# Kernel tuning notes

Hardware: AMD Instinct MI355X
Metric: run time of the kernel (lower is better)

## Reference

```python
import jax, jax.numpy as jnp
import numpy as np

B, T, C = 8, 2048, 1024
HEAD_SIZE = 64
HEAD_NUM = 0
NUM_HEADS = 16


def setup_inputs() -> dict:
    key = jax.random.key(0)
    k1, k2, k3, k4 = jax.random.split(key, 4)
    x = jax.random.normal(k1, (B, T, C), dtype=jnp.float32)
    s = C ** -0.5  # Linear init scale
    Wq = jax.random.normal(k2, (C, HEAD_SIZE), dtype=jnp.float32) * s
    Wk = jax.random.normal(k3, (C, HEAD_SIZE), dtype=jnp.float32) * s
    Wv = jax.random.normal(k4, (C, HEAD_SIZE), dtype=jnp.float32) * s
    return {"x": x, "Wq": Wq, "Wk": Wk, "Wv": Wv}


def reference(x, Wq, Wk, Wv):
    # single head of self-attention with ALiBi bias + causal mask (dropout in eval mode = identity)
    q = x @ Wq  # [B,T,H]
    k = x @ Wk  # [B,T,H]
    v = x @ Wv  # [B,T,H]
    scale = jnp.float32(HEAD_SIZE) ** -0.5
    t = jnp.arange(T)
    # base_bias[i,j] = j - i, scaled by per-head ALiBi slope
    slope = 2.0 ** (-8.0 * (HEAD_NUM + 1) / NUM_HEADS)
    m = (t[None, :] - t[:, None]).astype(jnp.float32) * slope  # [T,T]
    # note: bias is added BEFORE the 1/sqrt(d) scaling, as in the original
    scores = (jnp.einsum('bqh,bkh->bqk', q, k) + m) * scale  # [B,T,T]
    causal = t[None, :] <= t[:, None]  # [T,T] lower-triangular
    scores = jnp.where(causal, scores, -jnp.inf)
    attn = jax.nn.softmax(scores, axis=-1)
    out = jnp.einsum('bqk,bkh->bqh', attn, v)  # [B,T,H]
    return out
```

## Files before the change

### kernel.cpp

```cpp
#include <hip/hip_runtime.h>
#include <hip/hip_bf16.h>
#include <math.h>

#define B_ 8
#define T_ 2048
#define C_ 1024
#define H_ 64
#define M_ (B_*T_)

typedef __attribute__((ext_vector_type(8))) short bf16x8;
typedef __attribute__((ext_vector_type(4))) float floatx4;

static __device__ __forceinline__ unsigned short f2bf(float f) {
    union { float f; unsigned u; } v; v.f = f;
    unsigned r = v.u + 0x7fffu + ((v.u >> 16) & 1u);
    return (unsigned short)(r >> 16);
}
static __device__ __forceinline__ unsigned short f2bf_fast(float f) {
    union { float f; unsigned u; } v; v.f = f;
    return (unsigned short)((v.u + 0x8000u) >> 16);
}
static __device__ __forceinline__ unsigned pk2h(float lo, float hi) {
    union { float f; unsigned u; } a, b; a.f = lo; b.f = hi;
    return __builtin_amdgcn_perm(b.u + 0x8000u, a.u + 0x8000u, 0x07060302u);
}
static __device__ __forceinline__ bf16x8 cvt8(float4 f0, float4 f1) {
    union { uint4 u; bf16x8 v; } r;
    r.u.x = pk2h(f0.x, f0.y); r.u.y = pk2h(f0.z, f0.w);
    r.u.z = pk2h(f1.x, f1.y); r.u.w = pk2h(f1.z, f1.w);
    return r.v;
}
static __device__ __forceinline__ float fexp2(float x) {
#if defined(__has_builtin)
#if __has_builtin(__builtin_amdgcn_exp2f)
    return __builtin_amdgcn_exp2f(x);
#else
    return exp2f(x);
#endif
#else
    return exp2f(x);
#endif
}

#define MFMA(a,b,c) __builtin_amdgcn_mfma_f32_16x16x32_bf16((a),(b),(c),0,0,0)

__global__ __launch_bounds__(256) void wprep_kernel(
    const float* __restrict__ Wq, const float* __restrict__ Wk,
    const float* __restrict__ Wv, unsigned short* __restrict__ wt2)
{
    const int f    = blockIdx.x * 256 + threadIdx.x;
    const int nt   = f >> 11;
    const int kc   = (f >> 6) & 31;
    const int lane = f & 63;
    const int l15  = lane & 15, quad = lane >> 4;
    const int col  = nt * 16 + l15;
    const float* W = (col < 64) ? Wq : ((col < 128) ? Wk : Wv);
    const int   cw = col & 63;
    const float sc = (col < 64) ? 0.125f : 1.0f;
    unsigned short o[8];
    #pragma unroll
    for (int j = 0; j < 8; j++) {
        const int kk = kc * 32 + quad * 8 + j;
        o[j] = f2bf(W[(size_t)kk * 64 + cw] * sc);
    }
    *(uint4*)&wt2[(size_t)f * 8] = *(const uint4*)o;
}

__global__ __launch_bounds__(256) void qkv_kernel(
    const float* __restrict__ x, const unsigned short* __restrict__ wt2,
    unsigned short* __restrict__ qo, unsigned short* __restrict__ ko,
    unsigned short* __restrict__ vo)
{
    __shared__ __align__(16) unsigned short smem[32768];

    const int t    = threadIdx.x;
    const int w    = t >> 6;
    const int lane = t & 63;
    const int l15  = lane & 15;
    const int quad = lane >> 4;
    const int r0   = blockIdx.x * 32;

    {
        const int srow = t >> 3;
        const int g0   = t & 7;
        const float* xrow = x + (size_t)(r0 + srow) * C_;
        const int mt_  = srow >> 4;
        const int r15_ = srow & 15;
        const int ks_  = (g0 >> 2) & 1;
        const int qd_  = g0 & 3;
        unsigned short* dst = smem + (ks_ * 2 + mt_) * 512 + (qd_ * 16 + r15_) * 8;

        float4 cA0, cA1, cB0, cB1;
        cA0 = *(const float4*)(xrow + g0 * 8);
        cA1 = *(const float4*)(xrow + g0 * 8 + 4);
        #pragma unroll
        for (int i = 0; i < 16; i++) {
            if (i < 15) {
                cB0 = *(const float4*)(xrow + (i + 1) * 64 + g0 * 8);
                cB1 = *(const float4*)(xrow + (i + 1) * 64 + g0 * 8 + 4);
            }
            *(bf16x8*)(dst + i * 2048) = cvt8(cA0, cA1);
            cA0 = cB0; cA1 = cB1;
        }
    }
    __syncthreads();

    const unsigned short* wb = wt2 + (size_t)(w * 3) * 32 * 512 + lane * 8;

    floatx4 acc[2][3];
    #pragma unroll
    for (int mt = 0; mt < 2; mt++)
        #pragma unroll
        for (int nt = 0; nt < 3; nt++) acc[mt][nt] = (floatx4)(0.0f);

    bf16x8 wcur[6], wnxt[6];
    #pragma unroll
    for (int nt = 0; nt < 3; nt++)
        #pragma unroll
        for (int ks = 0; ks < 2; ks++)
            wcur[nt * 2 + ks] = *(const bf16x8*)(wb + (size_t)(nt * 32 + ks) * 512);

    #pragma unroll 2
    for (int c = 0; c < 16; c++) {
        if (c < 15) {
            #pragma unroll
            for (int nt = 0; nt < 3; nt++)
                #pragma unroll
                for (int ks = 0; ks < 2; ks++)
                    wnxt[nt * 2 + ks] = *(const bf16x8*)
                        (wb + (size_t)(nt * 32 + 2 * (c + 1) + ks) * 512);
        }
        #pragma unroll
        for (int ks = 0; ks < 2; ks++) {
            bf16x8 af[2];
            #pragma unroll
            for (int mt = 0; mt < 2; mt++)
                af[mt] = *(const bf16x8*)
                    (smem + ((c * 2 + ks) * 2 + mt) * 512 + lane * 8);
            #pragma unroll
            for (int mt = 0; mt < 2; mt++)
                #pragma unroll
                for (int nt = 0; nt < 3; nt++)
                    acc[mt][nt] = MFMA(af[mt], wcur[nt * 2 + ks], acc[mt][nt]);
        }
        if (c < 15) {
            #pragma unroll
            for (int i = 0; i < 6; i++) wcur[i] = wnxt[i];
        }
    }

    __syncthreads();
    #pragma unroll
    for (int mt = 0; mt < 2; mt++)
        #pragma unroll
        for (int nt = 0; nt < 3; nt++) {
            const int col = w * 48 + nt * 16 + l15;
            #pragma unroll
            for (int r = 0; r < 4; r++)
                smem[(mt * 16 + quad * 4 + r) * 200 + col] = f2bf(acc[mt][nt][r]);
        }
    __syncthreads();

    {
        const int row = t >> 3;
        const int oct = t & 7;
        *(uint4*)&qo[(size_t)(r0 + row) * 64 + oct * 8] =
            *(const uint4*)&smem[row * 200 + oct * 8];
        *(uint4*)&ko[(size_t)(r0 + row) * 64 + oct * 8] =
            *(const uint4*)&smem[row * 200 + 64 + oct * 8];
    }
    {
        const int h = t >> 2, ts = (t & 3) * 8;
        const int bb = r0 >> 11, tt = r0 & 2047;
        unsigned short tmp[8];
        #pragma unroll
        for (int j = 0; j < 8; j++) tmp[j] = smem[(ts + j) * 200 + 128 + h];
        *(uint4*)&vo[((size_t)bb * 64 + h) * 2048 + tt + ts] = *(uint4*)&tmp[0];
    }
}

#define L2E 1.4426950408889634f
#define BS2 0.12751743f
#define PSTR 76

__global__ __launch_bounds__(256, 3) void attn_kernel(
    const unsigned short* __restrict__ q,
    const unsigned short* __restrict__ k,
    const unsigned short* __restrict__ vT,
    float* __restrict__ out)
{
    __shared__ __align__(16) unsigned char smem[16384 + 512];
    unsigned short* pT  = (unsigned short*)smem;
    float*          Omg = (float*)smem;
    float*          mlg = (float*)(smem + 16384);

    const int t    = threadIdx.x;
    const int w    = t >> 6;
    const int lane = t & 63;
    const int l15  = lane & 15;
    const int quad = lane >> 4;
    const int b    = blockIdx.x & 7;
    const int qt   = 127 - (blockIdx.x >> 3);
    const int q0   = qt * 16;
    const size_t kb = (size_t)b * T_ * 64;

    bf16x8 qf[2];
    #pragma unroll
    for (int ks = 0; ks < 2; ks++)
        qf[ks] = *(const bf16x8*)
            &q[kb + (size_t)(q0 + l15) * 64 + ks * 32 + quad * 8];

    floatx4 O[4];
    float mrow[4], lrow[4];
    #pragma unroll
    for (int nt = 0; nt < 4; nt++) O[nt] = (floatx4)(0.0f);
    #pragma unroll
    for (int r = 0; r < 4; r++) { mrow[r] = -INFINITY; lrow[r] = 0.0f; }

    const int nsteps = (q0 + 16 + 63) >> 6;
    const int ns4    = (nsteps + 3) >> 2;
    const int sBeg   = w * ns4;
    const int sEnd   = min(sBeg + ns4, nsteps);
    unsigned short* pw = pT + w * 16 * PSTR;

    bf16x8 kf[4][2], vf[4][2];
    #define LOADK(dK, jj0)                                                     \
        { _Pragma("unroll")                                                    \
          for (int nt = 0; nt < 4; nt++)                                       \
              _Pragma("unroll")                                                \
              for (int ks = 0; ks < 2; ks++)                                   \
                  dK[nt][ks] = *(const bf16x8*)                                \
                      &k[kb + (size_t)((jj0) + nt*16 + l15)*64 + ks*32 + quad*8]; }
    #define LOADV(dV, jj0)                                                     \
        { _Pragma("unroll")                                                    \
          for (int nt = 0; nt < 4; nt++)                                       \
              _Pragma("unroll")                                                \
              for (int ks = 0; ks < 2; ks++)                                   \
                  dV[nt][ks] = *(const bf16x8*)                                \
                      &vT[((size_t)b*64 + nt*16 + l15)*2048 + (jj0) + ks*32 + quad*8]; }

    #define SMPART(MASKED)                                                     \
    {                                                                          \
        _Pragma("unroll")                                                      \
        for (int r = 0; r < 4; r++) {                                          \
            float xv[4];                                                       \
            _Pragma("unroll")                                                  \
            for (int nt = 0; nt < 4; nt++) {                                   \
                float v2 = fmaf(sc[nt][r], L2E, jn[nt]);                       \
                if (MASKED) {                                                  \
                    const int ig = q0 + quad * 4 + r;                          \
                    if (j0 + nt * 16 + l15 > ig) v2 = -INFINITY;               \
                }                                                              \
                xv[nt] = v2;                                                   \
            }                                                                  \
            float mloc = fmaxf(fmaxf(xv[0], xv[1]), fmaxf(xv[2], xv[3]));      \
            _Pragma("unroll")                                                  \
            for (int off = 1; off < 16; off <<= 1)                             \
                mloc = fmaxf(mloc, __shfl_xor(mloc, off));                     \
            const float mnew  = fmaxf(mrow[r], mloc);                          \
            const float alpha = fexp2(mrow[r] - mnew);                         \
            mrow[r] = mnew;                                                    \
            float ps = 0.0f;                                                   \
            _Pragma("unroll")                                                  \
            for (int nt = 0; nt < 4; nt++) {                                   \
                const float p = fexp2(xv[nt] - mnew);                          \
                ps += p;                                                       \
                pw[(quad * 4 + r) * PSTR + nt * 16 + l15] = f2bf_fast(p);      \
            }                                                                  \
            lrow[r] = lrow[r] * alpha + ps;                                    \
            _Pragma("unroll")                                                  \
            for (int nt = 0; nt < 4; nt++) O[nt][r] *= alpha;                  \
        }                                                                      \
    }

    if (sBeg < sEnd) LOADK(kf, sBeg * 64)

    for (int s = sBeg; s < sEnd; s++) {
        const int j0 = s * 64;

        floatx4 sc[4];
        #pragma unroll
        for (int nt = 0; nt < 4; nt++) {
            floatx4 z = (floatx4)(0.0f);
            z = MFMA(qf[0], kf[nt][0], z);
            z = MFMA(qf[1], kf[nt][1], z);
            sc[nt] = z;
        }

        LOADV(vf, j0)
        const bool more = (s + 1 < sEnd);
        if (more) LOADK(kf, (s + 1) * 64)

        const float jb = (float)(j0 + l15) * BS2;
        const float jn[4] = { jb, jb + 16.0f * BS2, jb + 32.0f * BS2,
                              jb + 48.0f * BS2 };
        if (s != nsteps - 1) SMPART(false) else SMPART(true);

        const bf16x8 pf0 = *(const bf16x8*)&pw[l15 * PSTR + quad * 8];
        const bf16x8 pf1 = *(const bf16x8*)&pw[l15 * PSTR + 32 + quad * 8];
        #pragma unroll
        for (int nt = 0; nt < 4; nt++) {
            O[nt] = MFMA(pf0, vf[nt][0], O[nt]);
            O[nt] = MFMA(pf1, vf[nt][1], O[nt]);
        }
    }
    #undef LOADK
    #undef LOADV
    #undef SMPART

    #pragma unroll
    for (int r = 0; r < 4; r++)
        #pragma unroll
        for (int off = 1; off < 16; off <<= 1)
            lrow[r] += __shfl_xor(lrow[r], off);

    __syncthreads();

    #pragma unroll
    for (int nt = 0; nt < 4; nt++)
        #pragma unroll
        for (int r = 0; r < 4; r++)
            Omg[w * 1024 + (quad * 4 + r) * 64 + nt * 16 + l15] = O[nt][r];
    if (l15 == 0) {
        #pragma unroll
        for (int r = 0; r < 4; r++) {
            mlg[w * 32 + quad * 4 + r]      = mrow[r];
            mlg[w * 32 + 16 + quad * 4 + r] = lrow[r];
        }
    }
    __syncthreads();

    {
        const int row = t >> 4;
        const int c4  = (t & 15) << 2;
        float mstar = -INFINITY;
        #pragma unroll
        for (int w2 = 0; w2 < 4; w2++)
            mstar = fmaxf(mstar, mlg[w2 * 32 + row]);
        floatx4 oa = (floatx4)(0.0f);
        float lsum = 0.0f;
        #pragma unroll
        for (int w2 = 0; w2 < 4; w2++) {
            const float wg = fexp2(mlg[w2 * 32 + row] - mstar);
            lsum += wg * mlg[w2 * 32 + 16 + row];
            oa += wg * *(const floatx4*)&Omg[w2 * 1024 + row * 64 + c4];
        }
        *(floatx4*)&out[kb + (size_t)(q0 + row) * 64 + c4] = oa * (1.0f / lsum);
    }
}

extern "C" void kernel_launch(void* const* d_in, const int* in_sizes, int n_in,
                              void* d_out, int out_size, void* d_ws, size_t ws_size,
                              hipStream_t stream) {
    (void)in_sizes; (void)n_in; (void)out_size; (void)ws_size;
    const float* x  = (const float*)d_in[0];
    const float* Wq = (const float*)d_in[1];
    const float* Wk = (const float*)d_in[2];
    const float* Wv = (const float*)d_in[3];
    float* out = (float*)d_out;

    unsigned short* wt2 = (unsigned short*)d_ws;
    unsigned short* qw  = wt2 + 196608;
    unsigned short* kw  = qw + (size_t)M_ * H_;
    unsigned short* vw  = kw + (size_t)M_ * H_;

    wprep_kernel<<<96, 256, 0, stream>>>(Wq, Wk, Wv, wt2);
    qkv_kernel<<<M_ / 32, 256, 0, stream>>>(x, wt2, qw, kw, vw);
    attn_kernel<<<B_ * 128, 256, 0, stream>>>(qw, kw, vw, out);
}
```

Measured before the change: 143.4 us.

## Transpose QK^T MFMA so softmax rows live per lane, cut shuffles

Result: no change. 143.0 us (-0.3%).

```diff
diff --git a/kernel.cpp b/kernel.cpp
--- a/kernel.cpp
+++ b/kernel.cpp
@@ -15,10 +15,6 @@
     union { float f; unsigned u; } v; v.f = f;
     unsigned r = v.u + 0x7fffu + ((v.u >> 16) & 1u);
     return (unsigned short)(r >> 16);
-}
-static __device__ __forceinline__ unsigned short f2bf_fast(float f) {
-    union { float f; unsigned u; } v; v.f = f;
-    return (unsigned short)((v.u + 0x8000u) >> 16);
 }
 static __device__ __forceinline__ unsigned pk2h(float lo, float hi) {
     union { float f; unsigned u; } a, b; a.f = lo; b.f = hi;
@@ -90,17 +86,19 @@
         const int qd_  = g0 & 3;
         unsigned short* dst = smem + (ks_ * 2 + mt_) * 512 + (qd_ * 16 + r15_) * 8;
 
-        float4 cA0, cA1, cB0, cB1;
-        cA0 = *(const float4*)(xrow + g0 * 8);
-        cA1 = *(const float4*)(xrow + g0 * 8 + 4);
+        float4 cb[4][2];
+        #pragma unroll
+        for (int i = 0; i < 3; i++) {
+            cb[i][0] = *(const float4*)(xrow + i * 64 + g0 * 8);
+            cb[i][1] = *(const float4*)(xrow + i * 64 + g0 * 8 + 4);
+        }
         #pragma unroll
         for (int i = 0; i < 16; i++) {
-            if (i < 15) {
-                cB0 = *(const float4*)(xrow + (i + 1) * 64 + g0 * 8);
-                cB1 = *(const float4*)(xrow + (i + 1) * 64 + g0 * 8 + 4);
+            if (i < 13) {
+                cb[(i + 3) & 3][0] = *(const float4*)(xrow + (i + 3) * 64 + g0 * 8);
+                cb[(i + 3) & 3][1] = *(const float4*)(xrow + (i + 3) * 64 + g0 * 8 + 4);
             }
-            *(bf16x8*)(dst + i * 2048) = cvt8(cA0, cA1);
-            cA0 = cB0; cA1 = cB1;
+            *(bf16x8*)(dst + i * 2048) = cvt8(cb[i & 3][0], cb[i & 3][1]);
         }
     }
     __syncthreads();
@@ -181,7 +179,7 @@
 
 #define L2E 1.4426950408889634f
 #define BS2 0.12751743f
-#define PSTR 76
+#define PSTR 72
 
 __global__ __launch_bounds__(256, 3) void attn_kernel(
     const unsigned short* __restrict__ q,
@@ -211,11 +209,16 @@
             &q[kb + (size_t)(q0 + l15) * 64 + ks * 32 + quad * 8];
 
     floatx4 O[4];
-    float mrow[4], lrow[4];
     #pragma unroll
     for (int nt = 0; nt < 4; nt++) O[nt] = (floatx4)(0.0f);
-    #pragma unroll
-    for (int r = 0; r < 4; r++) { mrow[r] = -INFINITY; lrow[r] = 0.0f; }
+    float mrow = -INFINITY, lrow = 0.0f;
+
+    float bconst[4][4];
+    #pragma unroll
+    for (int nt = 0; nt < 4; nt++)
+        #pragma unroll
+        for (int r = 0; r < 4; r++)
+            bconst[nt][r] = (float)(nt * 16 + quad * 4 + r) * BS2;
 
     const int nsteps = (q0 + 16 + 63) >> 6;
     const int ns4    = (nsteps + 3) >> 2;
@@ -241,78 +244,91 @@
 
     #define SMPART(MASKED)                                                     \
     {                                                                          \
+        float xv[4][4];                                                        \
+        const int qk2 = q0 + l15 - j0 - quad * 4;                              \
         _Pragma("unroll")                                                      \
-        for (int r = 0; r < 4; r++) {                                          \
-            float xv[4];                                                       \
+        for (int nt = 0; nt < 4; nt++)                                         \
             _Pragma("unroll")                                                  \
-            for (int nt = 0; nt < 4; nt++) {                                   \
-                float v2 = fmaf(sc[nt][r], L2E, jn[nt]);                       \
-                if (MASKED) {                                                  \
-                    const int ig = q0 + quad * 4 + r;                          \
-                    if (j0 + nt * 16 + l15 > ig) v2 = -INFINITY;               \
-                }                                                              \
-                xv[nt] = v2;                                                   \
+            for (int r = 0; r < 4; r++) {                                      \
+                float v2 = fmaf(sc[nt][r], L2E, bconst[nt][r]);                \
+                if (MASKED) { if (nt * 16 + r > qk2) v2 = -INFINITY; }         \
+                xv[nt][r] = v2;                                                \
             }                                                                  \
-            float mloc = fmaxf(fmaxf(xv[0], xv[1]), fmaxf(xv[2], xv[3]));      \
+                                            \
+        float m01 = fmaxf(fmaxf(xv[0][0], xv[0][1]), fmaxf(xv[0][2], xv[0][3]));\
+        float m11 = fmaxf(fmaxf(xv[1][0], xv[1][1]), fmaxf(xv[1][2], xv[1][3]));\
+        float m21 = fmaxf(fmaxf(xv[2][0], xv[2][1]), fmaxf(xv[2][2], xv[2][3]));\
+        float m31 = fmaxf(fmaxf(xv[3][0], xv[3][1]), fmaxf(xv[3][2], xv[3][3]));\
+        float mloc = fmaxf(fmaxf(m01, m11), fmaxf(m21, m31));                  \
+              \
+        mloc = fmaxf(mloc, __shfl_xor(mloc, 16));                              \
+        mloc = fmaxf(mloc, __shfl_xor(mloc, 32));                              \
+        const float mnew  = fmaxf(mrow, mloc + j0b);                           \
+        const float alpha = fexp2(mrow - mnew);                                \
+        mrow = mnew;                                                           \
+        const float msub = mnew - j0b;                                         \
+        float ps = 0.0f;                                                       \
+        _Pragma("unroll")                                                      \
+        for (int nt = 0; nt < 4; nt++) {                                       \
+            const float p0 = fexp2(xv[nt][0] - msub);                          \
+            const float p1 = fexp2(xv[nt][1] - msub);                          \
+            const float p2 = fexp2(xv[nt][2] - msub);                          \
+            const float p3 = fexp2(xv[nt][3] - msub);                          \
+            ps += (p0 + p1) + (p2 + p3);                                       \
+            union { unsigned u[2]; uint2 v; } pk;                              \
+            pk.u[0] = pk2h(p0, p1); pk.u[1] = pk2h(p2, p3);                    \
+            *(uint2*)&pw[l15 * PSTR + nt * 16 + quad * 4] = pk.v;              \
+        }                                                                      \
+        lrow = lrow * alpha + ps;                                              \
+                          \
+        float aT[4];                                                           \
+        _Pragma("unroll")                                                      \
+        for (int r = 0; r < 4; r++) aT[r] = __shfl(alpha, (quad << 2) + r);    \
+        _Pragma("unroll")                                                      \
+        for (int nt = 0; nt < 4; nt++)                                         \
             _Pragma("unroll")                                                  \
-            for (int off = 1; off < 16; off <<= 1)                             \
-                mloc = fmaxf(mloc, __shfl_xor(mloc, off));                     \
-            const float mnew  = fmaxf(mrow[r], mloc);                          \
-            const float alpha = fexp2(mrow[r] - mnew);                         \
-            mrow[r] = mnew;                                                    \
-            float ps = 0.0f;                                                   \
-            _Pragma("unroll")                                                  \
-            for (int nt = 0; nt < 4; nt++) {                                   \
-                const float p = fexp2(xv[nt] - mnew);                          \
-                ps += p;                                                       \
-                pw[(quad * 4 + r) * PSTR + nt * 16 + l15] = f2bf_fast(p);      \
-            }                                                                  \
-            lrow[r] = lrow[r] * alpha + ps;                                    \
-            _Pragma("unroll")                                                  \
-            for (int nt = 0; nt < 4; nt++) O[nt][r] *= alpha;                  \
-        }                                                                      \
+            for (int r = 0; r < 4; r++) O[nt][r] *= aT[r];                     \
     }
 
     if (sBeg < sEnd) LOADK(kf, sBeg * 64)
 
     for (int s = sBeg; s < sEnd; s++) {
         const int j0 = s * 64;
+        const float j0b = (float)j0 * BS2;
 
         floatx4 sc[4];
+        __builtin_amdgcn_s_setprio(1);
         #pragma unroll
         for (int nt = 0; nt < 4; nt++) {
             floatx4 z = (floatx4)(0.0f);
-            z = MFMA(qf[0], kf[nt][0], z);
-            z = MFMA(qf[1], kf[nt][1], z);
+            z = MFMA(kf[nt][0], qf[0], z);
+            z = MFMA(kf[nt][1], qf[1], z);
             sc[nt] = z;
         }
+        __builtin_amdgcn_s_setprio(0);
 
         LOADV(vf, j0)
         const bool more = (s + 1 < sEnd);
         if (more) LOADK(kf, (s + 1) * 64)
 
-        const float jb = (float)(j0 + l15) * BS2;
-        const float jn[4] = { jb, jb + 16.0f * BS2, jb + 32.0f * BS2,
-                              jb + 48.0f * BS2 };
         if (s != nsteps - 1) SMPART(false) else SMPART(true);
 
         const bf16x8 pf0 = *(const bf16x8*)&pw[l15 * PSTR + quad * 8];
         const bf16x8 pf1 = *(const bf16x8*)&pw[l15 * PSTR + 32 + quad * 8];
+        __builtin_amdgcn_s_setprio(1);
         #pragma unroll
         for (int nt = 0; nt < 4; nt++) {
             O[nt] = MFMA(pf0, vf[nt][0], O[nt]);
             O[nt] = MFMA(pf1, vf[nt][1], O[nt]);
         }
+        __builtin_amdgcn_s_setprio(0);
     }
     #undef LOADK
     #undef LOADV
     #undef SMPART
 
-    #pragma unroll
-    for (int r = 0; r < 4; r++)
-        #pragma unroll
-        for (int off = 1; off < 16; off <<= 1)
-            lrow[r] += __shfl_xor(lrow[r], off);
+    lrow += __shfl_xor(lrow, 16);
+    lrow += __shfl_xor(lrow, 32);
 
     __syncthreads();
 
@@ -321,12 +337,9 @@
         #pragma unroll
         for (int r = 0; r < 4; r++)
             Omg[w * 1024 + (quad * 4 + r) * 64 + nt * 16 + l15] = O[nt][r];
-    if (l15 == 0) {
-        #pragma unroll
-        for (int r = 0; r < 4; r++) {
-            mlg[w * 32 + quad * 4 + r]      = mrow[r];
-            mlg[w * 32 + 16 + quad * 4 + r] = lrow[r];
-        }
+    if (quad == 0) {
+        mlg[w * 32 + l15]      = mrow;
+        mlg[w * 32 + 16 + l15] = lrow;
     }
     __syncthreads();
 
```
